# Performance work log

Measured on AMD Instinct MI355X. Metric: run time of the kernel, lower is better.

Reference implementation:

```python
import jax, jax.numpy as jnp
import numpy as np

B, C, H, W = 64, 2048, 24, 8
NUM_IDS = 751


def setup_inputs() -> dict:
    key = jax.random.key(0)
    k1, k2, k3 = jax.random.split(key, 3)
    features_map = jax.random.normal(k1, (B, C, H, W), dtype=jnp.float32)
    classifier_weight = jax.random.normal(k2, (NUM_IDS, C), dtype=jnp.float32) * 0.02
    pids = jax.random.randint(k3, (B,), 0, NUM_IDS, dtype=jnp.int64)
    return {"features_map": features_map, "classifier_weight": classifier_weight, "pids": pids}


def reference(features_map, classifier_weight, pids):
    b, c, h, w = features_map.shape
    # gather one classifier weight row per sample: [B, C]
    wrows = classifier_weight[pids]
    # per-sample 1xC @ Cx(H*W) matmul -> heatmap [B, H, W]
    heat = jnp.einsum('bc,bchw->bhw', wrows, features_map)
    hflat = heat.reshape(b, h * w)
    mn = hflat.min(axis=-1, keepdims=True)
    mx = hflat.max(axis=-1, keepdims=True)
    # original: normalize only if max != 0
    hflat = jnp.where(mx != 0, (hflat - mn) / (mx - mn), hflat)
    heat = jax.lax.stop_gradient(hflat.reshape(b, h, w))  # heatmap is detached
    return features_map * heat[:, None, :, :]
```

## Files before the change

### kernel.cpp

```cpp
#include <hip/hip_runtime.h>

#define BB 64
#define CC 2048
#define HWN 192
#define HW4 48
#define NCHUNK 16
#define CCHUNK 128
#define CSLICE 32
#define NSLICE (CC / CSLICE)

__global__ void __launch_bounds__(192) heat_partial_kernel(
    const float* __restrict__ f,
    const float* __restrict__ w,
    const int* __restrict__ pids,
    float* __restrict__ partial)
{
    const int blk = blockIdx.x;
    const int b = blk >> 4;
    const int k = blk & (NCHUNK - 1);
    const int tid = threadIdx.x;
    const int hw4 = tid % HW4;
    const int cl  = tid / HW4;

    __shared__ float ws[CCHUNK];
    __shared__ __align__(16) float4 red[HWN];

    const int row = pids[b];
    if (tid < CCHUNK) ws[tid] = w[(size_t)row * CC + k * CCHUNK + tid];
    __syncthreads();

    const size_t base = ((size_t)b * CC + (size_t)k * CCHUNK) * HW4;
    const float4* fb4 = (const float4*)f + base;

    float4 acc = make_float4(0.f, 0.f, 0.f, 0.f);
#pragma unroll 8
    for (int c = cl; c < CCHUNK; c += 4) {
        float4 v = fb4[(size_t)c * HW4 + hw4];
        float wv = ws[c];
        acc.x = fmaf(wv, v.x, acc.x);
        acc.y = fmaf(wv, v.y, acc.y);
        acc.z = fmaf(wv, v.z, acc.z);
        acc.w = fmaf(wv, v.w, acc.w);
    }
    red[tid] = acc;
    __syncthreads();
    if (tid < HW4) {
        float4 a0 = red[tid], a1 = red[tid + 48], a2 = red[tid + 96], a3 = red[tid + 144];
        float4 s = make_float4(a0.x + a1.x + a2.x + a3.x,
                               a0.y + a1.y + a2.y + a3.y,
                               a0.z + a1.z + a2.z + a3.z,
                               a0.w + a1.w + a2.w + a3.w);
        ((float4*)partial)[(size_t)(b * NCHUNK + k) * HW4 + tid] = s;
    }
}

__global__ void __launch_bounds__(256) norm_scale_kernel(
    const float* __restrict__ f,
    const float* __restrict__ partial,
    float* __restrict__ out)
{
    const int blk = blockIdx.x;
    const int b  = blk / NSLICE;
    const int ck = blk % NSLICE;
    const int tid = threadIdx.x;

    __shared__ __align__(16) float vals[HWN];
    __shared__ __align__(16) float hl[HWN];
    __shared__ float s_mn, s_mx;

    float v = 0.f;
    if (tid < HWN) {
        const float* pb = partial + (size_t)b * NCHUNK * HWN + tid;
#pragma unroll
        for (int kk = 0; kk < NCHUNK; ++kk)
            v += pb[(size_t)kk * HWN];
        vals[tid] = v;
    }
    __syncthreads();

    if (tid < 64) {
        float m0 = vals[tid], m1 = vals[tid + 64], m2 = vals[tid + 128];
        float mn = fminf(m0, fminf(m1, m2));
        float mx = fmaxf(m0, fmaxf(m1, m2));
        for (int off = 32; off > 0; off >>= 1) {
            mn = fminf(mn, __shfl_down(mn, off));
            mx = fmaxf(mx, __shfl_down(mx, off));
        }
        if (tid == 0) { s_mn = mn; s_mx = mx; }
    }
    __syncthreads();

    if (tid < HWN) {
        const float mn = s_mn, mx = s_mx;
        hl[tid] = (mx != 0.f) ? (v - mn) / (mx - mn) : v;
    }
    __syncthreads();

    const size_t base = ((size_t)b * CC + (size_t)ck * CSLICE) * HW4;
    const float4* fb4 = (const float4*)f + base;
    float4* ob4 = (float4*)out + base;
    const float4* h4 = (const float4*)hl;

#pragma unroll
    for (int it = 0; it < (CSLICE * HW4) / 256; ++it) {
        const int idx = it * 256 + tid;
        const int hw4 = idx % HW4;
        const float4 hv = h4[hw4];
        float4 x = fb4[idx];
        x.x *= hv.x; x.y *= hv.y; x.z *= hv.z; x.w *= hv.w;
        ob4[idx] = x;
    }
}

extern "C" void kernel_launch(void* const* d_in, const int* in_sizes, int n_in,
                              void* d_out, int out_size, void* d_ws, size_t ws_size,
                              hipStream_t stream) {
    const float* features = (const float*)d_in[0];
    const float* weight   = (const float*)d_in[1];
    const int*   pids     = (const int*)d_in[2];
    float* out = (float*)d_out;
    float* partial = (float*)d_ws;

    heat_partial_kernel<<<BB * NCHUNK, HWN, 0, stream>>>(features, weight, pids, partial);
    norm_scale_kernel<<<BB * NSLICE, 256, 0, stream>>>(features, partial, out);
}
```

Before: 196.8 us.

## Accumulate heatmap with atomics and normalize in last-arriving block per sample

Each chunk block now atomically adds its partial heatmap into a per-sample buffer. A per-sample counter picks the last block, which computes the min/max normalisation once and writes the normalised heatmap to workspace. The scale kernel is restructured to 384 threads per block with 128 channels each, so every block reads a precomputed normalised heatmap instead of redoing the 16-way partial reduction and min/max. This adds a memset launch, float atomics that make the summation order nondeterministic, and a threadfence/counter protocol.

```diff
diff --git a/kernel.cpp b/kernel.cpp
--- a/kernel.cpp
+++ b/kernel.cpp
@@ -6,15 +6,23 @@
 #define HW4 48
 #define NCHUNK 16
 #define CCHUNK 128
-#define CSLICE 32
-#define NSLICE (CC / CSLICE)
+#define TPB 384
+#define CLANES 8
 
-__global__ void __launch_bounds__(192) heat_partial_kernel(
+#define HEAT_OFF  0
+#define CNT_OFF   (BB * HWN)
+#define HEATN_OFF (BB * HWN + BB)
+
+__global__ void __launch_bounds__(TPB) heat_atomic_kernel(
     const float* __restrict__ f,
     const float* __restrict__ w,
     const int* __restrict__ pids,
-    float* __restrict__ partial)
+    float* __restrict__ ws)
 {
+    float* heat  = ws + HEAT_OFF;
+    int*   cnt   = (int*)(ws + CNT_OFF);
+    float* heatN = ws + HEATN_OFF;
+
     const int blk = blockIdx.x;
     const int b = blk >> 4;
     const int k = blk & (NCHUNK - 1);
@@ -22,11 +30,13 @@
     const int hw4 = tid % HW4;
     const int cl  = tid / HW4;
 
-    __shared__ float ws[CCHUNK];
-    __shared__ __align__(16) float4 red[HWN];
+    __shared__ float wsm[CCHUNK];
+    __shared__ __align__(16) float4 red[TPB];
+    __shared__ int s_last;
+    __shared__ float s_mn, s_mx;
 
     const int row = pids[b];
-    if (tid < CCHUNK) ws[tid] = w[(size_t)row * CC + k * CCHUNK + tid];
+    if (tid < CCHUNK) wsm[tid] = w[(size_t)row * CC + (size_t)k * CCHUNK + tid];
     __syncthreads();
 
     const size_t base = ((size_t)b * CC + (size_t)k * CCHUNK) * HW4;
@@ -34,9 +44,9 @@
 
     float4 acc = make_float4(0.f, 0.f, 0.f, 0.f);
 #pragma unroll 8
-    for (int c = cl; c < CCHUNK; c += 4) {
+    for (int c = cl; c < CCHUNK; c += CLANES) {
         float4 v = fb4[(size_t)c * HW4 + hw4];
-        float wv = ws[c];
+        float wv = wsm[c];
         acc.x = fmaf(wv, v.x, acc.x);
         acc.y = fmaf(wv, v.y, acc.y);
         acc.z = fmaf(wv, v.z, acc.z);
@@ -45,39 +55,33 @@
     red[tid] = acc;
     __syncthreads();
     if (tid < HW4) {
-        float4 a0 = red[tid], a1 = red[tid + 48], a2 = red[tid + 96], a3 = red[tid + 144];
-        float4 s = make_float4(a0.x + a1.x + a2.x + a3.x,
-                               a0.y + a1.y + a2.y + a3.y,
-                               a0.z + a1.z + a2.z + a3.z,
-                               a0.w + a1.w + a2.w + a3.w);
-        ((float4*)partial)[(size_t)(b * NCHUNK + k) * HW4 + tid] = s;
+        float4 s = red[tid];
+#pragma unroll
+        for (int j = 1; j < CLANES; ++j) {
+            float4 a = red[tid + j * HW4];
+            s.x += a.x; s.y += a.y; s.z += a.z; s.w += a.w;
+        }
+        float* hp = heat + (size_t)b * HWN + hw4 * 4;
+        atomicAdd(hp + 0, s.x);
+        atomicAdd(hp + 1, s.y);
+        atomicAdd(hp + 2, s.z);
+        atomicAdd(hp + 3, s.w);
     }
-}
-
-__global__ void __launch_bounds__(256) norm_scale_kernel(
-    const float* __restrict__ f,
-    const float* __restrict__ partial,
-    float* __restrict__ out)
-{
-    const int blk = blockIdx.x;
-    const int b  = blk / NSLICE;
-    const int ck = blk % NSLICE;
-    const int tid = threadIdx.x;
-
-    __shared__ __align__(16) float vals[HWN];
-    __shared__ __align__(16) float hl[HWN];
-    __shared__ float s_mn, s_mx;
+    __syncthreads();
+    if (tid == 0) {
+        __threadfence();
+        int old = atomicAdd(&cnt[b], 1);
+        s_last = (old == NCHUNK - 1);
+    }
+    __syncthreads();
+    if (!s_last) return;
 
     float v = 0.f;
-    if (tid < HWN) {
-        const float* pb = partial + (size_t)b * NCHUNK * HWN + tid;
-#pragma unroll
-        for (int kk = 0; kk < NCHUNK; ++kk)
-            v += pb[(size_t)kk * HWN];
-        vals[tid] = v;
-    }
+    if (tid < HWN)
+        v = atomicAdd(&heat[(size_t)b * HWN + tid], 0.0f);
+    float* vals = (float*)red;
+    if (tid < HWN) vals[tid] = v;
     __syncthreads();
-
     if (tid < 64) {
         float m0 = vals[tid], m1 = vals[tid + 64], m2 = vals[tid + 128];
         float mn = fminf(m0, fminf(m1, m2));
@@ -89,23 +93,34 @@
         if (tid == 0) { s_mn = mn; s_mx = mx; }
     }
     __syncthreads();
-
     if (tid < HWN) {
         const float mn = s_mn, mx = s_mx;
-        hl[tid] = (mx != 0.f) ? (v - mn) / (mx - mn) : v;
+        heatN[(size_t)b * HWN + tid] = (mx != 0.f) ? (v - mn) / (mx - mn) : v;
     }
-    __syncthreads();
+}
 
-    const size_t base = ((size_t)b * CC + (size_t)ck * CSLICE) * HW4;
+__global__ void __launch_bounds__(TPB) scale_kernel(
+    const float* __restrict__ f,
+    const float* __restrict__ ws,
+    float* __restrict__ out)
+{
+    const float* heatN = ws + HEATN_OFF;
+    const int blk = blockIdx.x;
+    const int b = blk >> 4;
+    const int k = blk & (NCHUNK - 1);
+    const int tid = threadIdx.x;
+    const int hw4 = tid % HW4;
+    const int cl  = tid / HW4;
+
+    const float4 hv = ((const float4*)(heatN + (size_t)b * HWN))[hw4];
+
+    const size_t base = ((size_t)b * CC + (size_t)k * CCHUNK) * HW4;
     const float4* fb4 = (const float4*)f + base;
     float4* ob4 = (float4*)out + base;
-    const float4* h4 = (const float4*)hl;
 
-#pragma unroll
-    for (int it = 0; it < (CSLICE * HW4) / 256; ++it) {
-        const int idx = it * 256 + tid;
-        const int hw4 = idx % HW4;
-        const float4 hv = h4[hw4];
+#pragma unroll 8
+    for (int c = cl; c < CCHUNK; c += CLANES) {
+        const size_t idx = (size_t)c * HW4 + hw4;
         float4 x = fb4[idx];
         x.x *= hv.x; x.y *= hv.y; x.z *= hv.z; x.w *= hv.w;
         ob4[idx] = x;
@@ -119,8 +134,10 @@
     const float* weight   = (const float*)d_in[1];
     const int*   pids     = (const int*)d_in[2];
     float* out = (float*)d_out;
-    float* partial = (float*)d_ws;
+    float* ws  = (float*)d_ws;
 
-    heat_partial_kernel<<<BB * NCHUNK, HWN, 0, stream>>>(features, weight, pids, partial);
-    norm_scale_kernel<<<BB * NSLICE, 256, 0, stream>>>(features, partial, out);
+    hipMemsetAsync(d_ws, 0, (size_t)(BB * HWN + BB) * sizeof(float), stream);
+
+    heat_atomic_kernel<<<BB * NCHUNK, TPB, 0, stream>>>(features, weight, pids, ws);
+    scale_kernel<<<BB * NCHUNK, TPB, 0, stream>>>(features, ws, out);
 }
```

Result: slower. 243.5 us (+23.7%).
